# Kernel tuning notes

Hardware: AMD Instinct MI355X
Metric: run time of the kernel (lower is better)

The kernel has to match this reference:

```python
import jax, jax.numpy as jnp
import numpy as np


def setup_inputs() -> dict:
    key = jax.random.key(0)
    k1, k2, k3, k4 = jax.random.split(key, 4)
    B, D, C, N = 8192, 2048, 2048, 8
    x = jax.random.normal(k1, (B, D), dtype=jnp.float32)
    W = jax.random.normal(k2, (N, C, D), dtype=jnp.float32) * (1.0 / np.sqrt(D))
    b = jax.random.normal(k3, (N, C), dtype=jnp.float32) * 0.02
    factor = jnp.full((N,), 1.0 / N, dtype=jnp.float32)
    return {"x": x, "W": W, "b": b, "factor": factor}


def reference(x, W, b, factor):
    # Per-head linear: heads[b, n, c] = x @ W[n].T + b[n]
    heads = jnp.einsum("bd,ncd->bnc", x, W) + b[None, :, :]
    # Weighted sum over heads with canonical_factor (torch: cat(...,-1) @ factor)
    out = jnp.einsum("bnc,n->bc", heads, factor)
    return out
```

## Files before the change

kernel.cpp:

```cpp
#include <hip/hip_runtime.h>


#define MDIM 8192
#define KDIM 2048
#define NDIM 2048
#define NHEADS 8

#define BM 128
#define BN 128
#define BK 64

#define WBLKS 1024
#define XBLKS 1024
#define BBLKS 8

using bf16x8 = __attribute__((ext_vector_type(8))) short;
using f32x4  = __attribute__((ext_vector_type(4))) float;
using f4v    = __attribute__((ext_vector_type(4))) float;
using u16x8  = __attribute__((ext_vector_type(8))) unsigned short;

__device__ __forceinline__ unsigned short f2bf(float x) {
    unsigned int u = __float_as_uint(x);
    u += 0x7FFFu + ((u >> 16) & 1u);
    return (unsigned short)(u >> 16);
}

__device__ __forceinline__ void async_load16(const void* g, void* l) {
    __builtin_amdgcn_global_load_lds(
        (const __attribute__((address_space(1))) unsigned int*)g,
        (__attribute__((address_space(3))) unsigned int*)l,
        16, 0, 0);
}

__global__ __launch_bounds__(256) void prep_kernel(
        const float* __restrict__ x,
        const float* __restrict__ W,
        const float* __restrict__ b,
        const float* __restrict__ factor,
        unsigned short* __restrict__ xbf,
        unsigned short* __restrict__ Wbf,
        float* __restrict__ beff) {
    const int blk = blockIdx.x;
    const int tid = threadIdx.x;
    if (blk < WBLKS) {
        const size_t CD      = (size_t)NDIM * KDIM;
        const size_t tbase   = ((size_t)blk * 256 + tid) * 8;
        const size_t gstride = (size_t)WBLKS * 256 * 8;
        float f[NHEADS];
#pragma unroll
        for (int n = 0; n < NHEADS; ++n) f[n] = factor[n];
#pragma unroll
        for (int g = 0; g < 2; ++g) {
            const size_t i = tbase + (size_t)g * gstride;
            f4v v0[NHEADS], v1[NHEADS];
#pragma unroll
            for (int n = 0; n < NHEADS; ++n) {
                const float* p = W + (size_t)n * CD + i;
                v0[n] = *reinterpret_cast<const f4v*>(p);
                v1[n] = *reinterpret_cast<const f4v*>(p + 4);
            }
            float a0 = 0.f, a1 = 0.f, a2 = 0.f, a3 = 0.f;
            float a4 = 0.f, a5 = 0.f, a6 = 0.f, a7 = 0.f;
#pragma unroll
            for (int n = 0; n < NHEADS; ++n) {
                a0 += f[n] * v0[n].x; a1 += f[n] * v0[n].y;
                a2 += f[n] * v0[n].z; a3 += f[n] * v0[n].w;
                a4 += f[n] * v1[n].x; a5 += f[n] * v1[n].y;
                a6 += f[n] * v1[n].z; a7 += f[n] * v1[n].w;
            }
            u16x8 o;
            o[0] = f2bf(a0); o[1] = f2bf(a1); o[2] = f2bf(a2); o[3] = f2bf(a3);
            o[4] = f2bf(a4); o[5] = f2bf(a5); o[6] = f2bf(a6); o[7] = f2bf(a7);
            *reinterpret_cast<u16x8*>(Wbf + i) = o;
        }
    } else if (blk < WBLKS + XBLKS) {
        const size_t tbase   = ((size_t)(blk - WBLKS) * 256 + tid) * 8;
        const size_t gstride = (size_t)XBLKS * 256 * 8;
#pragma unroll
        for (int g = 0; g < 8; ++g) {
            const size_t i = tbase + (size_t)g * gstride;
            f4v v0 = *reinterpret_cast<const f4v*>(x + i);
            f4v v1 = *reinterpret_cast<const f4v*>(x + i + 4);
            u16x8 o;
            o[0] = f2bf(v0.x); o[1] = f2bf(v0.y); o[2] = f2bf(v0.z); o[3] = f2bf(v0.w);
            o[4] = f2bf(v1.x); o[5] = f2bf(v1.y); o[6] = f2bf(v1.z); o[7] = f2bf(v1.w);
            *reinterpret_cast<u16x8*>(xbf + i) = o;
        }
    } else {
        int c = (blk - WBLKS - XBLKS) * 256 + tid;
        float s = 0.f;
#pragma unroll
        for (int n = 0; n < NHEADS; ++n) s += factor[n] * b[(size_t)n * NDIM + c];
        beff[c] = s;
    }
}

__global__ __launch_bounds__(256) void gemm_bt_kernel(
    const unsigned short* __restrict__ A,
    const unsigned short* __restrict__ B,
    const float* __restrict__ bias,
    float* __restrict__ C)
{
    __shared__ unsigned short As[BM * BK];
    __shared__ unsigned short Bs[BN * BK];

    const int tid  = threadIdx.x;
    const int lane = tid & 63;
    const int w    = tid >> 6;
    const int m16  = lane & 15;
    const int quad = lane >> 4;

    const int bid = blockIdx.x;
    const int g   = bid >> 3;
    const int nt  = (bid & 7) * 2 + (g & 1);
    const int mt  = g >> 1;
    const int blockN0 = nt * BN;
    const int blockM0 = mt * BM;

    const int wr = (w >> 1) * 64;
    const int wc = (w & 1) * 64;

    const int srow = lane >> 3;
    const int scol = ((lane & 7) ^ srow) * 8;
    const unsigned short* aP[4];
    const unsigned short* bP[4];
    unsigned short* aL[4];
    unsigned short* bL[4];
#pragma unroll
    for (int i = 0; i < 4; ++i) {
        int r = i * 32 + w * 8;
        aP[i] = A + (size_t)(blockM0 + r + srow) * KDIM + scol;
        bP[i] = B + (size_t)(blockN0 + r + srow) * KDIM + scol;
        aL[i] = As + (size_t)r * BK;
        bL[i] = Bs + (size_t)r * BK;
    }

    f32x4 acc[4][4] = {};

    for (int k0 = 0; k0 < KDIM; k0 += BK) {
#pragma unroll
        for (int i = 0; i < 4; ++i) {
            async_load16(aP[i], aL[i]);
            async_load16(bP[i], bL[i]);
            aP[i] += BK; bP[i] += BK;
        }
        __syncthreads();

#pragma unroll
        for (int kk = 0; kk < BK; kk += 32) {
            bf16x8 af[4], bfr[4];
#pragma unroll
            for (int rt = 0; rt < 4; ++rt) {
                int row = wr + rt * 16 + m16;
                int gA = ((kk >> 3) + quad) ^ (row & 7);
                af[rt] = *reinterpret_cast<const bf16x8*>(&As[(size_t)row * BK + gA * 8]);
            }
#pragma unroll
            for (int ct = 0; ct < 4; ++ct) {
                int row = wc + ct * 16 + m16;
                int gB = ((kk >> 3) + quad) ^ (row & 7);
                bfr[ct] = *reinterpret_cast<const bf16x8*>(&Bs[(size_t)row * BK + gB * 8]);
            }
#pragma unroll
            for (int rt = 0; rt < 4; ++rt)
#pragma unroll
                for (int ct = 0; ct < 4; ++ct)
                    acc[rt][ct] = __builtin_amdgcn_mfma_f32_16x16x32_bf16(
                        af[rt], bfr[ct], acc[rt][ct], 0, 0, 0);
        }
        __syncthreads();
    }

    float bv[4];
#pragma unroll
    for (int ct = 0; ct < 4; ++ct) bv[ct] = bias[blockN0 + wc + ct * 16 + m16];
#pragma unroll
    for (int rt = 0; rt < 4; ++rt) {
        int row0 = blockM0 + wr + rt * 16 + quad * 4;
#pragma unroll
        for (int ct = 0; ct < 4; ++ct) {
            int col = blockN0 + wc + ct * 16 + m16;
#pragma unroll
            for (int r = 0; r < 4; ++r)
                C[(size_t)(row0 + r) * NDIM + col] = acc[rt][ct][r] + bv[ct];
        }
    }
}

extern "C" void kernel_launch(void* const* d_in, const int* in_sizes, int n_in,
                              void* d_out, int out_size, void* d_ws, size_t ws_size,
                              hipStream_t stream) {
    const float* x      = (const float*)d_in[0];
    const float* W      = (const float*)d_in[1];
    const float* b      = (const float*)d_in[2];
    const float* factor = (const float*)d_in[3];
    float* out = (float*)d_out;

    unsigned short* xbf  = (unsigned short*)d_ws;
    unsigned short* Wbf  = (unsigned short*)((char*)d_ws + 33554432);
    float*          beff = (float*)((char*)d_ws + 33554432 + 8388608);

    prep_kernel<<<dim3(WBLKS + XBLKS + BBLKS), dim3(256), 0, stream>>>(
        x, W, b, factor, xbf, Wbf, beff);
    gemm_bt_kernel<<<dim3(1024), dim3(256), 0, stream>>>(xbf, Wbf, beff, out);
}
```

Before: 332.1 us.

## Fuse x fp32-to-bf16 conversion into GEMM tile loads and split prep kernels

Removes the separate pass that converted x to bf16 in workspace. The GEMM now reads fp32 x directly, converts it with packed v_cvt_pk_bf16_f32 instructions, and writes it to LDS through registers. The W and bias preparation move into two separate kernels. This cuts a full read and write of x plus the bf16 re-read. In exchange, the A-tile loads become synchronous register loads of twice the bytes inside the main loop, which can expose global memory latency in the GEMM.

```diff
diff --git a/kernel.cpp b/kernel.cpp
--- a/kernel.cpp
+++ b/kernel.cpp
@@ -11,7 +11,6 @@
 #define BK 64
 
 #define WBLKS 1024
-#define XBLKS 1024
 #define BBLKS 8
 
 using bf16x8 = __attribute__((ext_vector_type(8))) short;
@@ -23,6 +22,12 @@
     unsigned int u = __float_as_uint(x);
     u += 0x7FFFu + ((u >> 16) & 1u);
     return (unsigned short)(u >> 16);
+}
+
+__device__ __forceinline__ unsigned int cvt_pk_bf16(float lo, float hi) {
+    unsigned int r;
+    asm("v_cvt_pk_bf16_f32 %0, %1, %2" : "=v"(r) : "v"(lo), "v"(hi));
+    return r;
 }
 
 __device__ __forceinline__ void async_load16(const void* g, void* l) {
@@ -32,71 +37,55 @@
         16, 0, 0);
 }
 
-__global__ __launch_bounds__(256) void prep_kernel(
-        const float* __restrict__ x,
+__global__ __launch_bounds__(256) void prep_w_kernel(
         const float* __restrict__ W,
+        const float* __restrict__ factor,
+        unsigned short* __restrict__ Wbf) {
+    const size_t CD      = (size_t)NDIM * KDIM;
+    const size_t tbase   = ((size_t)blockIdx.x * 256 + threadIdx.x) * 8;
+    const size_t gstride = (size_t)WBLKS * 256 * 8;
+    float f[NHEADS];
+#pragma unroll
+    for (int n = 0; n < NHEADS; ++n) f[n] = factor[n];
+#pragma unroll
+    for (int g = 0; g < 2; ++g) {
+        const size_t i = tbase + (size_t)g * gstride;
+        f4v v0[NHEADS], v1[NHEADS];
+#pragma unroll
+        for (int n = 0; n < NHEADS; ++n) {
+            const float* p = W + (size_t)n * CD + i;
+            v0[n] = *reinterpret_cast<const f4v*>(p);
+            v1[n] = *reinterpret_cast<const f4v*>(p + 4);
+        }
+        float a0 = 0.f, a1 = 0.f, a2 = 0.f, a3 = 0.f;
+        float a4 = 0.f, a5 = 0.f, a6 = 0.f, a7 = 0.f;
+#pragma unroll
+        for (int n = 0; n < NHEADS; ++n) {
+            a0 += f[n] * v0[n].x; a1 += f[n] * v0[n].y;
+            a2 += f[n] * v0[n].z; a3 += f[n] * v0[n].w;
+            a4 += f[n] * v1[n].x; a5 += f[n] * v1[n].y;
+            a6 += f[n] * v1[n].z; a7 += f[n] * v1[n].w;
+        }
+        u16x8 o;
+        o[0] = f2bf(a0); o[1] = f2bf(a1); o[2] = f2bf(a2); o[3] = f2bf(a3);
+        o[4] = f2bf(a4); o[5] = f2bf(a5); o[6] = f2bf(a6); o[7] = f2bf(a7);
+        *reinterpret_cast<u16x8*>(Wbf + i) = o;
+    }
+}
+
+__global__ __launch_bounds__(256) void prep_bias_kernel(
         const float* __restrict__ b,
         const float* __restrict__ factor,
-        unsigned short* __restrict__ xbf,
-        unsigned short* __restrict__ Wbf,
         float* __restrict__ beff) {
-    const int blk = blockIdx.x;
-    const int tid = threadIdx.x;
-    if (blk < WBLKS) {
-        const size_t CD      = (size_t)NDIM * KDIM;
-        const size_t tbase   = ((size_t)blk * 256 + tid) * 8;
-        const size_t gstride = (size_t)WBLKS * 256 * 8;
-        float f[NHEADS];
-#pragma unroll
-        for (int n = 0; n < NHEADS; ++n) f[n] = factor[n];
-#pragma unroll
-        for (int g = 0; g < 2; ++g) {
-            const size_t i = tbase + (size_t)g * gstride;
-            f4v v0[NHEADS], v1[NHEADS];
-#pragma unroll
-            for (int n = 0; n < NHEADS; ++n) {
-                const float* p = W + (size_t)n * CD + i;
-                v0[n] = *reinterpret_cast<const f4v*>(p);
-                v1[n] = *reinterpret_cast<const f4v*>(p + 4);
-            }
-            float a0 = 0.f, a1 = 0.f, a2 = 0.f, a3 = 0.f;
-            float a4 = 0.f, a5 = 0.f, a6 = 0.f, a7 = 0.f;
-#pragma unroll
-            for (int n = 0; n < NHEADS; ++n) {
-                a0 += f[n] * v0[n].x; a1 += f[n] * v0[n].y;
-                a2 += f[n] * v0[n].z; a3 += f[n] * v0[n].w;
-                a4 += f[n] * v1[n].x; a5 += f[n] * v1[n].y;
-                a6 += f[n] * v1[n].z; a7 += f[n] * v1[n].w;
-            }
-            u16x8 o;
-            o[0] = f2bf(a0); o[1] = f2bf(a1); o[2] = f2bf(a2); o[3] = f2bf(a3);
-            o[4] = f2bf(a4); o[5] = f2bf(a5); o[6] = f2bf(a6); o[7] = f2bf(a7);
-            *reinterpret_cast<u16x8*>(Wbf + i) = o;
-        }
-    } else if (blk < WBLKS + XBLKS) {
-        const size_t tbase   = ((size_t)(blk - WBLKS) * 256 + tid) * 8;
-        const size_t gstride = (size_t)XBLKS * 256 * 8;
-#pragma unroll
-        for (int g = 0; g < 8; ++g) {
-            const size_t i = tbase + (size_t)g * gstride;
-            f4v v0 = *reinterpret_cast<const f4v*>(x + i);
-            f4v v1 = *reinterpret_cast<const f4v*>(x + i + 4);
-            u16x8 o;
-            o[0] = f2bf(v0.x); o[1] = f2bf(v0.y); o[2] = f2bf(v0.z); o[3] = f2bf(v0.w);
-            o[4] = f2bf(v1.x); o[5] = f2bf(v1.y); o[6] = f2bf(v1.z); o[7] = f2bf(v1.w);
-            *reinterpret_cast<u16x8*>(xbf + i) = o;
-        }
-    } else {
-        int c = (blk - WBLKS - XBLKS) * 256 + tid;
-        float s = 0.f;
-#pragma unroll
-        for (int n = 0; n < NHEADS; ++n) s += factor[n] * b[(size_t)n * NDIM + c];
-        beff[c] = s;
-    }
+    int c = blockIdx.x * 256 + threadIdx.x;
+    float s = 0.f;
+#pragma unroll
+    for (int n = 0; n < NHEADS; ++n) s += factor[n] * b[(size_t)n * NDIM + c];
+    beff[c] = s;
 }
 
 __global__ __launch_bounds__(256) void gemm_bt_kernel(
-    const unsigned short* __restrict__ A,
+    const float* __restrict__ X,
     const unsigned short* __restrict__ B,
     const float* __restrict__ bias,
     float* __restrict__ C)
@@ -122,16 +111,16 @@
 
     const int srow = lane >> 3;
     const int scol = ((lane & 7) ^ srow) * 8;
-    const unsigned short* aP[4];
+    const float*          xP[4];
     const unsigned short* bP[4];
-    unsigned short* aL[4];
-    unsigned short* bL[4];
+    unsigned short*       aW[4];
+    unsigned short*       bL[4];
 #pragma unroll
     for (int i = 0; i < 4; ++i) {
         int r = i * 32 + w * 8;
-        aP[i] = A + (size_t)(blockM0 + r + srow) * KDIM + scol;
+        xP[i] = X + (size_t)(blockM0 + r + srow) * KDIM + scol;
         bP[i] = B + (size_t)(blockN0 + r + srow) * KDIM + scol;
-        aL[i] = As + (size_t)r * BK;
+        aW[i] = As + (size_t)r * BK + lane * 8;
         bL[i] = Bs + (size_t)r * BK;
     }
 
@@ -140,9 +129,20 @@
     for (int k0 = 0; k0 < KDIM; k0 += BK) {
 #pragma unroll
         for (int i = 0; i < 4; ++i) {
-            async_load16(aP[i], aL[i]);
             async_load16(bP[i], bL[i]);
-            aP[i] += BK; bP[i] += BK;
+            bP[i] += BK;
+        }
+#pragma unroll
+        for (int i = 0; i < 4; ++i) {
+            f4v v0 = *reinterpret_cast<const f4v*>(xP[i]);
+            f4v v1 = *reinterpret_cast<const f4v*>(xP[i] + 4);
+            xP[i] += BK;
+            uint4 o;
+            o.x = cvt_pk_bf16(v0.x, v0.y);
+            o.y = cvt_pk_bf16(v0.z, v0.w);
+            o.z = cvt_pk_bf16(v1.x, v1.y);
+            o.w = cvt_pk_bf16(v1.z, v1.w);
+            *reinterpret_cast<uint4*>(aW[i]) = o;
         }
         __syncthreads();
 
@@ -196,11 +196,10 @@
     const float* factor = (const float*)d_in[3];
     float* out = (float*)d_out;
 
-    unsigned short* xbf  = (unsigned short*)d_ws;
-    unsigned short* Wbf  = (unsigned short*)((char*)d_ws + 33554432);
-    float*          beff = (float*)((char*)d_ws + 33554432 + 8388608);
-
-    prep_kernel<<<dim3(WBLKS + XBLKS + BBLKS), dim3(256), 0, stream>>>(
-        x, W, b, factor, xbf, Wbf, beff);
-    gemm_bt_kernel<<<dim3(1024), dim3(256), 0, stream>>>(xbf, Wbf, beff, out);
-}
+    unsigned short* Wbf  = (unsigned short*)d_ws;
+    float*          beff = (float*)((char*)d_ws + 8388608);
+
+    prep_w_kernel<<<dim3(WBLKS), dim3(256), 0, stream>>>(W, factor, Wbf);
+    prep_bias_kernel<<<dim3(BBLKS), dim3(256), 0, stream>>>(b, factor, beff);
+    gemm_bt_kernel<<<dim3(1024), dim3(256), 0, stream>>>(x, Wbf, beff, out);
+}
```

Result: slower. 355.0 us (+6.9%).
